# Kernel tuning notes

Measured on AMD Instinct MI355X. Metric: run time of the kernel, lower is better.

The kernel has to match this reference:

```python
import jax, jax.numpy as jnp
import numpy as np

LEAK = 0.2
EPS = 1e-8


def _mod_conv(x, style, weight):
    # x: [B,C,H,W], style: [B,C], weight: [O,C,k,k]
    b, c, h, w = x.shape
    o, _, k, _ = weight.shape
    # per-sample modulation + demodulation (StyleGAN2 style)
    wmod = weight[None] * (style[:, None, :, None, None] + 1.0)  # [B,O,C,k,k]
    d = jax.lax.rsqrt(jnp.sum(wmod * wmod, axis=(2, 3, 4), keepdims=True) + EPS)
    wmod = wmod * d
    pad = (k - 1) // 2  # same padding for stride=1, dilation=1
    xg = x.reshape(1, b * c, h, w)
    wg = wmod.reshape(b * o, c, k, k)
    y = jax.lax.conv_general_dilated(
        xg, wg, window_strides=(1, 1), padding=[(pad, pad), (pad, pad)],
        dimension_numbers=('NCHW', 'OIHW', 'NCHW'), feature_group_count=b)
    return y.reshape(b, o, h, w)


def setup_inputs() -> dict:
    key = jax.random.key(0)
    ks = jax.random.split(key, 8)
    B, LAT, CIN, F, H, W = 8, 512, 256, 256, 64, 64
    K = 3
    kaiming = lambda k, shape, fan_in: jax.random.normal(k, shape, jnp.float32) * np.sqrt(2.0 / fan_in)
    return {
        'x': jax.random.normal(ks[0], (B, CIN, H, W), jnp.float32),
        'istyle': jax.random.normal(ks[1], (B, LAT), jnp.float32),
        'ws1': jax.random.normal(ks[2], (CIN, LAT), jnp.float32) * (1.0 / np.sqrt(LAT)),
        'bs1': jnp.zeros((CIN,), jnp.float32),
        'conv1_w': kaiming(ks[3], (F, CIN, K, K), CIN * K * K),
        'ws2': jax.random.normal(ks[4], (F, LAT), jnp.float32) * (1.0 / np.sqrt(LAT)),
        'bs2': jnp.zeros((F,), jnp.float32),
        'conv2_w': kaiming(ks[5], (F, F, K, K), F * K * K),
    }


def reference(x, istyle, ws1, bs1, conv1_w, ws2, bs2, conv2_w):
    b, c, h, w = x.shape
    # bilinear upsample x2, align_corners=False (half-pixel centers)
    x = jax.image.resize(x, (b, c, 2 * h, 2 * w), method='bilinear')
    s1 = istyle @ ws1.T + bs1
    x = _mod_conv(x, s1, conv1_w)
    x = jax.nn.leaky_relu(x, LEAK)
    s2 = istyle @ ws2.T + bs2
    x = _mod_conv(x, s2, conv2_w)
    return jax.nn.leaky_relu(x, LEAK)
```

## Files before the change

kernel.cpp:

```cpp
#include <hip/hip_runtime.h>

typedef __bf16 bf16x8 __attribute__((ext_vector_type(8)));
typedef float f32x4 __attribute__((ext_vector_type(4)));


#define GLDS(gsrc, ldst) __builtin_amdgcn_global_load_lds( \
    (const __attribute__((address_space(1))) unsigned int*)(gsrc), \
    (__attribute__((address_space(3))) unsigned int*)(ldst), 16, 0, 0)

#define MFMA(a, b, c) __builtin_amdgcn_mfma_f32_16x16x32_bf16((a), (b), (c), 0, 0, 0)

__global__ void style_kernel(const float* __restrict__ istyle,
                             const float* __restrict__ ws1, const float* __restrict__ bs1,
                             const float* __restrict__ ws2, const float* __restrict__ bs2,
                             float* __restrict__ sbuf) {
    int b = blockIdx.x;
    int which = blockIdx.y;
    int c = threadIdx.x;
    const float* ws = which ? ws2 : ws1;
    const float* bs = which ? bs2 : bs1;
    __shared__ float st[512];
    for (int i = threadIdx.x; i < 512; i += 256) st[i] = istyle[b * 512 + i];
    __syncthreads();
    float acc = bs[c];
    const float* wr = ws + (size_t)c * 512;
    for (int l = 0; l < 512; ++l) acc += st[l] * wr[l];
    sbuf[((size_t)which * 8 + b) * 256 + c] = acc;
}

__global__ void modw_kernel(const float* __restrict__ w, const float* __restrict__ s,
                            __bf16* __restrict__ wm) {
    int wv = threadIdx.x >> 6, lane = threadIdx.x & 63;
    int idx = blockIdx.x * 4 + wv;
    int b = idx >> 8, o = idx & 255;
    int c0 = lane * 4;
    const float* wr = w + ((size_t)o * 256 + c0) * 9;
    const float* sb = s + (size_t)b * 256 + c0;
    float v[36];
    float ss = 0.f;
#pragma unroll
    for (int cc = 0; cc < 4; ++cc) {
        float sm = sb[cc] + 1.0f;
#pragma unroll
        for (int t = 0; t < 9; ++t) {
            float x = wr[cc * 9 + t] * sm;
            v[cc * 9 + t] = x;
            ss += x * x;
        }
    }
#pragma unroll
    for (int off = 32; off > 0; off >>= 1) ss += __shfl_xor(ss, off);
    float d = rsqrtf(ss + 1e-8f);
    __bf16* wp = wm + ((size_t)(b * 256 + o) * 9) * 256 + c0;
#pragma unroll
    for (int t = 0; t < 9; ++t) {
        union { __bf16 h[4]; uint2 u; } pk;
#pragma unroll
        for (int cc = 0; cc < 4; ++cc) pk.h[cc] = (__bf16)(v[cc * 9 + t] * d);
        *(uint2*)(wp + (size_t)t * 256) = pk.u;
    }
}

__global__ void zeropad_kernel(__bf16* __restrict__ xu, __bf16* __restrict__ y1) {
    int p0 = blockIdx.x * 8;
    int b  = blockIdx.y;
    __bf16* buf = blockIdx.z ? y1 : xu;
    int p = p0 + (threadIdx.x >> 5);
    if (p >= 516) return;
    int chunk = threadIdx.x & 31;
    int y, x;
    if (p < 130)      { y = 0;           x = p; }
    else if (p < 260) { y = 129;         x = p - 130; }
    else if (p < 388) { y = p - 260 + 1; x = 0; }
    else              { y = p - 388 + 1; x = 129; }
    uint4 z = make_uint4(0, 0, 0, 0);
    *(uint4*)(buf + (((size_t)b * 130 + y) * 130 + x) * 256 + chunk * 8) = z;
}

__global__ void upsample_kernel(const float* __restrict__ x, __bf16* __restrict__ xu) {
    int ct = blockIdx.x;
    int y  = blockIdx.y;
    int b  = blockIdx.z;
    int c0 = ct * 32;
    __shared__ float up[32 * 132];
    int tid = threadIdx.x;

    int j = y >> 1;
    int y0, y1; float wy0, wy1;
    if (y & 1) { y0 = j; y1 = (j + 1 < 64) ? j + 1 : 63; wy0 = 0.75f; wy1 = 0.25f; }
    else       { y0 = (j - 1 >= 0) ? j - 1 : 0; y1 = j; wy0 = 0.25f; wy1 = 0.75f; }

    int c  = tid >> 3;
    int xs = (tid & 7) * 16;
    const float* row0 = x + ((size_t)(b * 256 + c0 + c) * 64 + y0) * 64;
    const float* row1 = x + ((size_t)(b * 256 + c0 + c) * 64 + y1) * 64;
#pragma unroll
    for (int k = 0; k < 16; ++k) {
        int xo = xs + k;
        int i = xo >> 1;
        int x0, x1; float wx0, wx1;
        if (xo & 1) { x0 = i; x1 = (i + 1 < 64) ? i + 1 : 63; wx0 = 0.75f; wx1 = 0.25f; }
        else        { x0 = (i - 1 >= 0) ? i - 1 : 0; x1 = i; wx0 = 0.25f; wx1 = 0.75f; }
        float v0 = wx0 * row0[x0] + wx1 * row0[x1];
        float v1 = wx0 * row1[x0] + wx1 * row1[x1];
        up[c * 132 + xo] = wy0 * v0 + wy1 * v1;
    }
    __syncthreads();
    int xo = tid >> 1, half = tid & 1;
    union { __bf16 v[8]; uint4 u; } pk;
#pragma unroll
    for (int g = 0; g < 2; ++g) {
#pragma unroll
        for (int i = 0; i < 8; ++i)
            pk.v[i] = (__bf16)up[(half * 16 + g * 8 + i) * 132 + xo];
        *(uint4*)(xu + (((size_t)(b * 130) + y + 1) * 130 + xo + 1) * 256 + c0 + half * 16 + g * 8) = pk.u;
    }
}

template <int PHASE>
__global__ __launch_bounds__(256, 2) void conv_kernel(
    const __bf16* __restrict__ in,
    const __bf16* __restrict__ wmall,
    float* __restrict__ outf,
    __bf16* __restrict__ outb) {
    __shared__ __attribute__((aligned(128))) char smem[65536];
    __bf16* const sA = (__bf16*)smem;
    __bf16* const sB = (__bf16*)(smem + 32768);
    const int tid  = threadIdx.x;
    const int bid  = blockIdx.x;
    const int swz  = (bid & 7) * 256 + (bid >> 3);
    const int b    = swz >> 8;
    const int rem  = swz & 255;
    const int yrow = rem >> 1;
    const int om   = (rem & 1) * 128;
    const int lane = tid & 63;
    const int wv   = tid >> 6;
    const int wo   = (wv >> 1) * 64;
    const int wn   = (wv & 1) * 64;
    const int arow = lane & 15;
    const int cgb  = lane >> 4;
    const int lr   = lane >> 3;
    const int lc   = lane & 7;
    const int swz8 = (lc ^ lr) * 8;
    const __bf16* wm_b = wmall + (size_t)(b * 256 + om) * 2304;

    size_t aOff[4], bOff[4];
    int dst[4];
#pragma unroll
    for (int q = 0; q < 4; ++q) {
        int r = q * 32 + wv * 8 + lr;
        aOff[q] = (size_t)r * 2304 + swz8;
        bOff[q] = ((size_t)((b * 130 + yrow) * 130 + r)) * 256 + swz8;
        dst[q]  = (q * 32 + wv * 8) * 64;
    }

    f32x4 acc[4][4] = {};

#pragma unroll
    for (int q = 0; q < 4; ++q) {
        GLDS(wm_b + aOff[q], sA + dst[q]);
        GLDS(in   + bOff[q], sB + dst[q]);
    }
    asm volatile("s_waitcnt vmcnt(0)" ::: "memory");
    __builtin_amdgcn_s_barrier();
    asm volatile("" ::: "memory");

    for (int t = 0; t < 36; ++t) {
        const __bf16* Ac = sA + (t & 1) * 8192;
        const __bf16* Bc = sB + (t & 1) * 8192;
        __bf16* An = sA + ((t + 1) & 1) * 8192;
        __bf16* Bn = sB + ((t + 1) & 1) * 8192;
        if (t < 35) {
            const int nt   = t + 1;
            const int ncb  = nt / 9;
            const int ntap = nt - 9 * ncb;
            const int nc0  = ncb * 64;
            const int nky  = ntap / 3, nkx = ntap - 3 * nky;
            const size_t boff_t = (size_t)((nky * 130 + nkx) * 256 + nc0);
            const size_t aoff_t = (size_t)(ntap * 256 + nc0);
#pragma unroll
            for (int q = 0; q < 4; ++q) {
                GLDS(wm_b + aOff[q] + aoff_t, An + dst[q]);
                GLDS(in   + bOff[q] + boff_t, Bn + dst[q]);
            }
        }
        bf16x8 bfr[4][2], af[4][2];
#pragma unroll
        for (int j = 0; j < 4; ++j) {
            int rb = wn + j * 16 + arow;
            const char* bp = (const char*)Bc + rb * 128;
            bfr[j][0] = *(const bf16x8*)(bp + ((cgb ^ (rb & 7)) * 16));
            bfr[j][1] = *(const bf16x8*)(bp + (((cgb + 4) ^ (rb & 7)) * 16));
        }
#pragma unroll
        for (int m = 0; m < 4; ++m) {
            int ra = wo + m * 16 + arow;
            const char* ap = (const char*)Ac + ra * 128;
            af[m][0] = *(const bf16x8*)(ap + ((cgb ^ (ra & 7)) * 16));
            af[m][1] = *(const bf16x8*)(ap + (((cgb + 4) ^ (ra & 7)) * 16));
        }
        __builtin_amdgcn_s_setprio(1);
#pragma unroll
        for (int m = 0; m < 4; ++m)
#pragma unroll
            for (int j = 0; j < 4; ++j) {
                acc[m][j] = MFMA(af[m][0], bfr[j][0], acc[m][j]);
                acc[m][j] = MFMA(af[m][1], bfr[j][1], acc[m][j]);
            }
        __builtin_amdgcn_s_setprio(0);
        asm volatile("s_waitcnt vmcnt(0)" ::: "memory");
        __builtin_amdgcn_s_barrier();
        asm volatile("" ::: "memory");
    }

    __builtin_amdgcn_sched_barrier(0);
    __syncthreads();

    if (PHASE == 1) {
        __bf16* const ot = (__bf16*)smem;
        const int cg = lane >> 4;
#pragma unroll
        for (int m = 0; m < 4; ++m)
#pragma unroll
            for (int j = 0; j < 4; ++j) {
                int n  = wn + j * 16 + arow;
                int ob = (wo + m * 16 + cg * 4) * 2;
                union { __bf16 v[4]; uint2 u; } pk;
#pragma unroll
                for (int r = 0; r < 4; ++r) {
                    float v = acc[m][j][r];
                    pk.v[r] = (__bf16)((v > 0.f) ? v : 0.2f * v);
                }
                *(uint2*)((char*)ot + n * 256 + (ob ^ ((n & 7) << 4))) = pk.u;
            }
        __syncthreads();
        const int p4  = lane >> 4;
        const int c16 = lane & 15;
#pragma unroll
        for (int it = 0; it < 8; ++it) {
            int n = wv * 32 + it * 4 + p4;
            uint4 v = *(const uint4*)((const char*)ot + n * 256 + ((c16 * 16) ^ ((n & 7) << 4)));
            *(uint4*)(outb + (((size_t)(b * 130) + yrow + 1) * 130 + n + 1) * 256 + om + c16 * 8) = v;
        }
    } else {
#pragma unroll
        for (int m = 0; m < 4; ++m)
#pragma unroll
            for (int j = 0; j < 4; ++j) {
                int o_base = om + wo + m * 16 + (lane >> 4) * 4;
                int n      = wn + j * 16 + (lane & 15);
#pragma unroll
                for (int r = 0; r < 4; ++r) {
                    float v = acc[m][j][r];
                    v = (v > 0.f) ? v : 0.2f * v;
                    outf[((size_t)(b * 256 + o_base + r) * 128 + yrow) * 128 + n] = v;
                }
            }
    }
}

extern "C" void kernel_launch(void* const* d_in, const int* in_sizes, int n_in,
                              void* d_out, int out_size, void* d_ws, size_t ws_size,
                              hipStream_t stream) {
    const float* x      = (const float*)d_in[0];
    const float* istyle = (const float*)d_in[1];
    const float* ws1    = (const float*)d_in[2];
    const float* bs1    = (const float*)d_in[3];
    const float* w1     = (const float*)d_in[4];
    const float* ws2    = (const float*)d_in[5];
    const float* bs2    = (const float*)d_in[6];
    const float* w2     = (const float*)d_in[7];
    float* out = (float*)d_out;

    char* ws = (char*)d_ws;
    __bf16* xu_p = (__bf16*)(ws);
    __bf16* y1_p = (__bf16*)(ws + 69222400);
    __bf16* wm   = (__bf16*)(ws + 138444800);
    float*  sbuf = (float*)(ws + 147881984);

    style_kernel<<<dim3(8, 2), 256, 0, stream>>>(istyle, ws1, bs1, ws2, bs2, sbuf);
    zeropad_kernel<<<dim3(65, 8, 2), 256, 0, stream>>>(xu_p, y1_p);
    upsample_kernel<<<dim3(8, 128, 8), 256, 0, stream>>>(x, xu_p);
    modw_kernel<<<dim3(512), 256, 0, stream>>>(w1, sbuf, wm);
    conv_kernel<1><<<dim3(2048), 256, 0, stream>>>(xu_p, wm, nullptr, y1_p);
    modw_kernel<<<dim3(512), 256, 0, stream>>>(w2, sbuf + 2048, wm);
    conv_kernel<2><<<dim3(2048), 256, 0, stream>>>(y1_p, wm, out, nullptr);
}
```

Before: 398.4 us.

## Enlarge conv tile to all 256 outputs per row, halve K-step, full-row upsample

The conv kernel now computes all 256 output channels for an image row per block (256x128 tile, 8x4 MFMA accumulators per wave), using 32-channel K steps over 72 iterations with a new LDS swizzle. Each input row is loaded once rather than twice, and the grid is halved. The upsample kernel now writes a whole row across all channels as bf16 in LDS, then stores it contiguously. The trade-off is more accumulator registers (launch bounds still request 2 blocks/CU), fewer blocks in flight, and twice as many barriers per K.

```diff
diff --git a/kernel.cpp b/kernel.cpp
--- a/kernel.cpp
+++ b/kernel.cpp
@@ -77,12 +77,11 @@
     *(uint4*)(buf + (((size_t)b * 130 + y) * 130 + x) * 256 + chunk * 8) = z;
 }
 
-__global__ void upsample_kernel(const float* __restrict__ x, __bf16* __restrict__ xu) {
-    int ct = blockIdx.x;
-    int y  = blockIdx.y;
-    int b  = blockIdx.z;
-    int c0 = ct * 32;
-    __shared__ float up[32 * 132];
+__global__ __launch_bounds__(256) void upsample_kernel(const float* __restrict__ x,
+                                                       __bf16* __restrict__ xu) {
+    int y = blockIdx.x;
+    int b = blockIdx.y;
+    __shared__ __bf16 orow[128 * 256];
     int tid = threadIdx.x;
 
     int j = y >> 1;
@@ -92,29 +91,28 @@
 
     int c  = tid >> 3;
     int xs = (tid & 7) * 16;
-    const float* row0 = x + ((size_t)(b * 256 + c0 + c) * 64 + y0) * 64;
-    const float* row1 = x + ((size_t)(b * 256 + c0 + c) * 64 + y1) * 64;
-#pragma unroll
-    for (int k = 0; k < 16; ++k) {
-        int xo = xs + k;
-        int i = xo >> 1;
-        int x0, x1; float wx0, wx1;
-        if (xo & 1) { x0 = i; x1 = (i + 1 < 64) ? i + 1 : 63; wx0 = 0.75f; wx1 = 0.25f; }
-        else        { x0 = (i - 1 >= 0) ? i - 1 : 0; x1 = i; wx0 = 0.25f; wx1 = 0.75f; }
-        float v0 = wx0 * row0[x0] + wx1 * row0[x1];
-        float v1 = wx0 * row1[x0] + wx1 * row1[x1];
-        up[c * 132 + xo] = wy0 * v0 + wy1 * v1;
+    for (int ct = 0; ct < 8; ++ct) {
+        int cc = ct * 32 + c;
+        const float* row0 = x + ((size_t)(b * 256 + cc) * 64 + y0) * 64;
+        const float* row1 = x + ((size_t)(b * 256 + cc) * 64 + y1) * 64;
+#pragma unroll
+        for (int k = 0; k < 16; ++k) {
+            int xo = xs + k;
+            int i = xo >> 1;
+            int x0, x1; float wx0, wx1;
+            if (xo & 1) { x0 = i; x1 = (i + 1 < 64) ? i + 1 : 63; wx0 = 0.75f; wx1 = 0.25f; }
+            else        { x0 = (i - 1 >= 0) ? i - 1 : 0; x1 = i; wx0 = 0.25f; wx1 = 0.75f; }
+            float v0 = wx0 * row0[x0] + wx1 * row0[x1];
+            float v1 = wx0 * row1[x0] + wx1 * row1[x1];
+            orow[xo * 256 + cc] = (__bf16)(wy0 * v0 + wy1 * v1);
+        }
     }
     __syncthreads();
-    int xo = tid >> 1, half = tid & 1;
-    union { __bf16 v[8]; uint4 u; } pk;
-#pragma unroll
-    for (int g = 0; g < 2; ++g) {
-#pragma unroll
-        for (int i = 0; i < 8; ++i)
-            pk.v[i] = (__bf16)up[(half * 16 + g * 8 + i) * 132 + xo];
-        *(uint4*)(xu + (((size_t)(b * 130) + y + 1) * 130 + xo + 1) * 256 + c0 + half * 16 + g * 8) = pk.u;
-    }
+    uint4* dst = (uint4*)(xu + (((size_t)(b * 130) + y + 1) * 130 + 1) * 256);
+    const uint4* src = (const uint4*)orow;
+#pragma unroll
+    for (int it = 0; it < 16; ++it)
+        dst[it * 256 + tid] = src[it * 256 + tid];
 }
 
 template <int PHASE>
@@ -124,94 +122,69 @@
     float* __restrict__ outf,
     __bf16* __restrict__ outb) {
     __shared__ __attribute__((aligned(128))) char smem[65536];
-    __bf16* const sA = (__bf16*)smem;
-    __bf16* const sB = (__bf16*)(smem + 32768);
     const int tid  = threadIdx.x;
     const int bid  = blockIdx.x;
-    const int swz  = (bid & 7) * 256 + (bid >> 3);
-    const int b    = swz >> 8;
-    const int rem  = swz & 255;
-    const int yrow = rem >> 1;
-    const int om   = (rem & 1) * 128;
+    const int swz  = (bid & 7) * 128 + (bid >> 3);
+    const int b    = swz >> 7;
+    const int yrow = swz & 127;
     const int lane = tid & 63;
     const int wv   = tid >> 6;
-    const int wo   = (wv >> 1) * 64;
+    const int wo   = (wv >> 1) * 128;
     const int wn   = (wv & 1) * 64;
     const int arow = lane & 15;
     const int cgb  = lane >> 4;
-    const int lr   = lane >> 3;
-    const int lc   = lane & 7;
-    const int swz8 = (lc ^ lr) * 8;
-    const __bf16* wm_b = wmall + (size_t)(b * 256 + om) * 2304;
-
-    size_t aOff[4], bOff[4];
-    int dst[4];
-#pragma unroll
-    for (int q = 0; q < 4; ++q) {
-        int r = q * 32 + wv * 8 + lr;
-        aOff[q] = (size_t)r * 2304 + swz8;
-        bOff[q] = ((size_t)((b * 130 + yrow) * 130 + r)) * 256 + swz8;
-        dst[q]  = (q * 32 + wv * 8) * 64;
-    }
-
-    f32x4 acc[4][4] = {};
-
-#pragma unroll
-    for (int q = 0; q < 4; ++q) {
-        GLDS(wm_b + aOff[q], sA + dst[q]);
-        GLDS(in   + bOff[q], sB + dst[q]);
-    }
+    const int xsw  = (cgb ^ ((arow >> 1) & 3)) * 16;
+    const int srow   = wv * 16 + (lane >> 2);
+    const int chunkS = (lane & 3) ^ ((lane >> 3) & 3);
+    const __bf16* wm_b = wmall + (size_t)b * 256 * 2304;
+    const __bf16* arow_base = wm_b + (size_t)srow * 2304 + chunkS * 8;
+    const __bf16* brow_base = in + ((size_t)((b * 130 + yrow) * 130 + srow)) * 256 + chunkS * 8;
+    const int ldsA = (wv * 16) * 32;
+    const int ldsB = (wv * 16) * 32;
+
+    f32x4 acc[8][4] = {};
+
+#define STAGE(tt, buf)                                                          \
+    {   const int tap = (tt) % 9, cb = (tt) / 9;                                \
+        const size_t aoff = (size_t)(tap * 256 + cb * 32);                      \
+        const size_t boff = (size_t)(((tap / 3) * 130 + (tap % 3)) * 256 + cb * 32); \
+        __bf16* Ad = (__bf16*)smem + (buf) * 8192 + ldsA;                       \
+        __bf16* Bd = (__bf16*)(smem + 32768) + (buf) * 4096 + ldsB;             \
+        _Pragma("unroll")                                                       \
+        for (int q = 0; q < 4; ++q)                                             \
+            GLDS(arow_base + aoff + (size_t)q * 64 * 2304, Ad + q * 64 * 32);   \
+        _Pragma("unroll")                                                       \
+        for (int q = 0; q < 2; ++q)                                             \
+            GLDS(brow_base + boff + (size_t)q * 64 * 256, Bd + q * 64 * 32);    \
+    }
+
+    STAGE(0, 0);
     asm volatile("s_waitcnt vmcnt(0)" ::: "memory");
     __builtin_amdgcn_s_barrier();
     asm volatile("" ::: "memory");
 
-    for (int t = 0; t < 36; ++t) {
-        const __bf16* Ac = sA + (t & 1) * 8192;
-        const __bf16* Bc = sB + (t & 1) * 8192;
-        __bf16* An = sA + ((t + 1) & 1) * 8192;
-        __bf16* Bn = sB + ((t + 1) & 1) * 8192;
-        if (t < 35) {
-            const int nt   = t + 1;
-            const int ncb  = nt / 9;
-            const int ntap = nt - 9 * ncb;
-            const int nc0  = ncb * 64;
-            const int nky  = ntap / 3, nkx = ntap - 3 * nky;
-            const size_t boff_t = (size_t)((nky * 130 + nkx) * 256 + nc0);
-            const size_t aoff_t = (size_t)(ntap * 256 + nc0);
-#pragma unroll
-            for (int q = 0; q < 4; ++q) {
-                GLDS(wm_b + aOff[q] + aoff_t, An + dst[q]);
-                GLDS(in   + bOff[q] + boff_t, Bn + dst[q]);
-            }
-        }
-        bf16x8 bfr[4][2], af[4][2];
-#pragma unroll
-        for (int j = 0; j < 4; ++j) {
-            int rb = wn + j * 16 + arow;
-            const char* bp = (const char*)Bc + rb * 128;
-            bfr[j][0] = *(const bf16x8*)(bp + ((cgb ^ (rb & 7)) * 16));
-            bfr[j][1] = *(const bf16x8*)(bp + (((cgb + 4) ^ (rb & 7)) * 16));
-        }
-#pragma unroll
-        for (int m = 0; m < 4; ++m) {
-            int ra = wo + m * 16 + arow;
-            const char* ap = (const char*)Ac + ra * 128;
-            af[m][0] = *(const bf16x8*)(ap + ((cgb ^ (ra & 7)) * 16));
-            af[m][1] = *(const bf16x8*)(ap + (((cgb + 4) ^ (ra & 7)) * 16));
-        }
+    for (int t = 0; t < 72; ++t) {
+        const int cur = t & 1;
+        if (t < 71) STAGE(t + 1, cur ^ 1);
+        const char* Ab = smem + cur * 16384 + (wo + arow) * 64 + xsw;
+        const char* Bb = smem + 32768 + cur * 8192 + (wn + arow) * 64 + xsw;
+        bf16x8 af[8], bfr[4];
+#pragma unroll
+        for (int jj = 0; jj < 4; ++jj) bfr[jj] = *(const bf16x8*)(Bb + jj * 1024);
+#pragma unroll
+        for (int m = 0; m < 8; ++m) af[m] = *(const bf16x8*)(Ab + m * 1024);
         __builtin_amdgcn_s_setprio(1);
 #pragma unroll
-        for (int m = 0; m < 4; ++m)
-#pragma unroll
-            for (int j = 0; j < 4; ++j) {
-                acc[m][j] = MFMA(af[m][0], bfr[j][0], acc[m][j]);
-                acc[m][j] = MFMA(af[m][1], bfr[j][1], acc[m][j]);
-            }
+        for (int m = 0; m < 8; ++m)
+#pragma unroll
+            for (int jj = 0; jj < 4; ++jj)
+                acc[m][jj] = MFMA(af[m], bfr[jj], acc[m][jj]);
         __builtin_amdgcn_s_setprio(0);
         asm volatile("s_waitcnt vmcnt(0)" ::: "memory");
         __builtin_amdgcn_s_barrier();
         asm volatile("" ::: "memory");
     }
+#undef STAGE
 
     __builtin_amdgcn_sched_barrier(0);
     __syncthreads();
@@ -220,38 +193,38 @@
         __bf16* const ot = (__bf16*)smem;
         const int cg = lane >> 4;
 #pragma unroll
-        for (int m = 0; m < 4; ++m)
-#pragma unroll
-            for (int j = 0; j < 4; ++j) {
-                int n  = wn + j * 16 + arow;
+        for (int m = 0; m < 8; ++m)
+#pragma unroll
+            for (int jj = 0; jj < 4; ++jj) {
+                int n  = wn + jj * 16 + arow;
                 int ob = (wo + m * 16 + cg * 4) * 2;
                 union { __bf16 v[4]; uint2 u; } pk;
 #pragma unroll
                 for (int r = 0; r < 4; ++r) {
-                    float v = acc[m][j][r];
+                    float v = acc[m][jj][r];
                     pk.v[r] = (__bf16)((v > 0.f) ? v : 0.2f * v);
                 }
-                *(uint2*)((char*)ot + n * 256 + (ob ^ ((n & 7) << 4))) = pk.u;
+                *(uint2*)((char*)ot + n * 512 + (ob ^ ((n & 7) << 4))) = pk.u;
             }
         __syncthreads();
-        const int p4  = lane >> 4;
-        const int c16 = lane & 15;
-#pragma unroll
-        for (int it = 0; it < 8; ++it) {
-            int n = wv * 32 + it * 4 + p4;
-            uint4 v = *(const uint4*)((const char*)ot + n * 256 + ((c16 * 16) ^ ((n & 7) << 4)));
-            *(uint4*)(outb + (((size_t)(b * 130) + yrow + 1) * 130 + n + 1) * 256 + om + c16 * 8) = v;
+        const int half = lane >> 5;
+        const int l32  = lane & 31;
+#pragma unroll
+        for (int it = 0; it < 16; ++it) {
+            int n = wv * 32 + it * 2 + half;
+            uint4 v = *(const uint4*)((const char*)ot + n * 512 + ((l32 * 16) ^ ((n & 7) << 4)));
+            *(uint4*)(outb + (((size_t)(b * 130) + yrow + 1) * 130 + n + 1) * 256 + l32 * 8) = v;
         }
     } else {
 #pragma unroll
-        for (int m = 0; m < 4; ++m)
-#pragma unroll
-            for (int j = 0; j < 4; ++j) {
-                int o_base = om + wo + m * 16 + (lane >> 4) * 4;
-                int n      = wn + j * 16 + (lane & 15);
+        for (int m = 0; m < 8; ++m)
+#pragma unroll
+            for (int jj = 0; jj < 4; ++jj) {
+                int o_base = wo + m * 16 + (lane >> 4) * 4;
+                int n      = wn + jj * 16 + (lane & 15);
 #pragma unroll
                 for (int r = 0; r < 4; ++r) {
-                    float v = acc[m][j][r];
+                    float v = acc[m][jj][r];
                     v = (v > 0.f) ? v : 0.2f * v;
                     outf[((size_t)(b * 256 + o_base + r) * 128 + yrow) * 128 + n] = v;
                 }
@@ -280,9 +253,9 @@
 
     style_kernel<<<dim3(8, 2), 256, 0, stream>>>(istyle, ws1, bs1, ws2, bs2, sbuf);
     zeropad_kernel<<<dim3(65, 8, 2), 256, 0, stream>>>(xu_p, y1_p);
-    upsample_kernel<<<dim3(8, 128, 8), 256, 0, stream>>>(x, xu_p);
+    upsample_kernel<<<dim3(128, 8), 256, 0, stream>>>(x, xu_p);
     modw_kernel<<<dim3(512), 256, 0, stream>>>(w1, sbuf, wm);
-    conv_kernel<1><<<dim3(2048), 256, 0, stream>>>(xu_p, wm, nullptr, y1_p);
+    conv_kernel<1><<<dim3(1024), 256, 0, stream>>>(xu_p, wm, nullptr, y1_p);
     modw_kernel<<<dim3(512), 256, 0, stream>>>(w2, sbuf + 2048, wm);
-    conv_kernel<2><<<dim3(2048), 256, 0, stream>>>(y1_p, wm, out, nullptr);
-}
+    conv_kernel<2><<<dim3(1024), 256, 0, stream>>>(y1_p, wm, out, nullptr);
+}
```

New measurement: 427.5 us. 7.3% more time.
